# Kernel tuning notes

Measured on AMD Instinct MI355X. Metric: run time of the kernel, lower is better.

The kernel has to match this reference:

```python
import jax, jax.numpy as jnp
import numpy as np

N_NODES = 50000
N_EDGES = 800000
IN_CH = 128
HEADS = 2
OUT_CH = 64
NEG_SLOPE = 0.2


def setup_inputs() -> dict:
    key = jax.random.key(0)
    ks = jax.random.split(key, 8)
    x = jax.random.normal(ks[0], (N_NODES, IN_CH), dtype=jnp.float32)
    # edges with no self-loops (module strips them anyway before re-adding)
    src = jax.random.randint(ks[1], (N_EDGES,), 0, N_NODES)
    off = jax.random.randint(ks[2], (N_EDGES,), 1, N_NODES)
    dst = (src + off) % N_NODES
    edge_index = jnp.stack([src, dst]).astype(jnp.int64)
    sc = 1.0 / np.sqrt(IN_CH)
    Wl = jax.random.normal(ks[3], (IN_CH, HEADS * OUT_CH), dtype=jnp.float32) * sc
    att_l = jax.random.normal(ks[4], (1, HEADS, OUT_CH), dtype=jnp.float32) * 0.1
    att_r = jax.random.normal(ks[5], (1, HEADS, OUT_CH), dtype=jnp.float32) * 0.1
    Wout = jax.random.normal(ks[6], (HEADS * OUT_CH, OUT_CH), dtype=jnp.float32) * (1.0 / np.sqrt(HEADS * OUT_CH))
    bias = jnp.zeros((OUT_CH,), dtype=jnp.float32)
    return {"x": x, "edge_index": edge_index, "Wl": Wl, "att_l": att_l,
            "att_r": att_r, "Wout": Wout, "bias": bias}


def reference(x, edge_index, Wl, att_l, att_r, Wout, bias):
    N = x.shape[0]
    H, C = att_l.shape[1], att_l.shape[2]
    # input edges have no self-loops; module removes then re-adds them
    loops = jnp.arange(N, dtype=edge_index.dtype)
    src = jnp.concatenate([edge_index[0], loops])  # j (source / neighbor)
    dst = jnp.concatenate([edge_index[1], loops])  # i (target / aggregation index)
    # shared lin_l == lin_r projection -> [N, H, C]
    xh = (x @ Wl).reshape(N, H, C)
    alpha_l = jnp.sum(xh * att_l, axis=-1)  # [N, H]
    alpha_r = jnp.sum(xh * att_r, axis=-1)  # [N, H]
    # per-edge attention logits: alpha_j + alpha_i, then LeakyReLU
    e = jax.nn.leaky_relu(alpha_l[src] + alpha_r[dst], negative_slope=NEG_SLOPE)  # [E, H]
    # segment softmax over destination nodes (numerically stable)
    emax = jax.ops.segment_max(e, dst, num_segments=N)
    emax = jnp.where(jnp.isfinite(emax), emax, 0.0)
    ex = jnp.exp(e - emax[dst])
    denom = jax.ops.segment_sum(ex, dst, num_segments=N)
    alpha = ex / (denom[dst] + 1e-16)  # matches PyG softmax eps
    # weighted scatter-add aggregation of source features
    msg = xh[src] * alpha[:, :, None]                # [E, H, C]
    out = jax.ops.segment_sum(msg, dst, num_segments=N)  # [N, H, C]
    # concat heads -> output projection + bias (concat=True, bias=True path)
    out = out.reshape(N, H * C) @ Wout + bias
    return out
```

## Files before the change

### kernel.cpp

```cpp
#include <hip/hip_runtime.h>
#include <hip/hip_fp16.h>

#define NEG_SLOPE 0.2f

static __device__ __forceinline__ unsigned short f2bf(float f) {
    unsigned u = __float_as_uint(f);
    unsigned r = (u + 0x7fffu + ((u >> 16) & 1u)) >> 16;
    return (unsigned short)r;
}
static __device__ __forceinline__ float bflo(unsigned z) {
    return __uint_as_float((z & 0xffffu) << 16);
}
static __device__ __forceinline__ float bfhi(unsigned z) {
    return __uint_as_float(z & 0xffff0000u);
}

#define PREP_B 66

__global__ __launch_bounds__(256) void prep_count_kernel(
    const float* __restrict__ Wl, const float* __restrict__ Wout,
    const float* __restrict__ attL, const float* __restrict__ attR,
    float* __restrict__ Wc, float* __restrict__ avec,
    const int* __restrict__ ei, int E, int Etot, int* __restrict__ cnt)
{
    int bid = blockIdx.x;
    if (bid < PREP_B) {
        int idx = bid * 256 + threadIdx.x;
        if (idx < 128 * 128) {
            int k = idx >> 7, c = idx & 127;
            int h = c >> 6, cc = c & 63;
            const float* wl = Wl + k * 128 + h * 64;
            const float* wo = Wout + (h * 64) * 64 + cc;
            float s = 0.f;
#pragma unroll 8
            for (int m = 0; m < 64; ++m) s += wl[m] * wo[m * 64];
            Wc[k * 128 + c] = s;
        } else if (idx < 128 * 128 + 512) {
            int r = idx - 128 * 128;
            int k = r >> 2, t = r & 3;
            int h = t & 1;
            const float* av = ((t < 2) ? attL : attR) + h * 64;
            const float* wl = Wl + k * 128 + h * 64;
            float s = 0.f;
#pragma unroll 8
            for (int m = 0; m < 64; ++m) s += wl[m] * av[m];
            avec[k * 4 + t] = s;
        }
    } else {
        int e = (bid - PREP_B) * 256 + threadIdx.x;
        if (e >= Etot) return;
        int dst = (e < E) ? ei[E + e] : (e - E);
        atomicAdd(&cnt[dst], 1);
    }
}

__global__ __launch_bounds__(256, 4) void zproj_scan_kernel(
    const float* __restrict__ x, const float* __restrict__ Wc,
    const float* __restrict__ avec, int N, int ZB,
    unsigned short* __restrict__ Z, float* __restrict__ AL, float* __restrict__ AR,
    const int* __restrict__ cnt, int* __restrict__ off, int* __restrict__ chs)
{
    __shared__ float xs[64 * 136];
    __shared__ float avs[128 * 4];
    const int tid = threadIdx.x;

    if ((int)blockIdx.x >= ZB) {
        int blk = blockIdx.x - ZB;
        int* s = (int*)xs;
        int i = blk * 256 + tid;
        int v = (i < N) ? cnt[i] : 0;
        s[tid] = v; __syncthreads();
#pragma unroll
        for (int o = 1; o < 256; o <<= 1) {
            int add = (tid >= o) ? s[tid - o] : 0;
            __syncthreads();
            s[tid] += add;
            __syncthreads();
        }
        if (i < N) off[i] = s[tid] - v;
        if (tid == 255) chs[blk] = s[255];
        return;
    }

    const int row0 = blockIdx.x * 64;
    const float4* x4 = (const float4*)x;
#pragma unroll
    for (int it = 0; it < 8; ++it) {
        int f4 = it * 256 + tid;
        int r = f4 >> 5, kq = f4 & 31;
        int rsrc = row0 + r; if (rsrc >= N) rsrc = N - 1;
        float4 v = x4[(size_t)rsrc * 32 + kq];
        *(float4*)&xs[r * 136 + kq * 4] = v;
    }
    if (tid < 128) *(float4*)&avs[tid * 4] = *(const float4*)&avec[tid * 4];
    __syncthreads();

    const int cg = tid & 31;
    const int rg = tid >> 5;
    const int c0 = cg * 4, r0 = rg * 8;
    float acc[8][4] = {};
    const float* wp = Wc + c0;
    for (int kc = 0; kc < 32; ++kc) {
        int k = kc * 4;
        float4 w0 = *(const float4*)&wp[(k + 0) * 128];
        float4 w1 = *(const float4*)&wp[(k + 1) * 128];
        float4 w2 = *(const float4*)&wp[(k + 2) * 128];
        float4 w3 = *(const float4*)&wp[(k + 3) * 128];
#pragma unroll
        for (int i = 0; i < 8; ++i) {
            float4 xv = *(const float4*)&xs[(r0 + i) * 136 + k];
            acc[i][0] += xv.x * w0.x + xv.y * w1.x + xv.z * w2.x + xv.w * w3.x;
            acc[i][1] += xv.x * w0.y + xv.y * w1.y + xv.z * w2.y + xv.w * w3.y;
            acc[i][2] += xv.x * w0.z + xv.y * w1.z + xv.z * w2.z + xv.w * w3.z;
            acc[i][3] += xv.x * w0.w + xv.y * w1.w + xv.z * w2.w + xv.w * w3.w;
        }
    }
#pragma unroll
    for (int i = 0; i < 8; ++i) {
        int row = row0 + r0 + i;
        if (row < N) {
            ushort4 zz;
            zz.x = f2bf(acc[i][0]); zz.y = f2bf(acc[i][1]);
            zz.z = f2bf(acc[i][2]); zz.w = f2bf(acc[i][3]);
            *(ushort4*)(Z + (size_t)row * 128 + c0) = zz;
        }
    }
    {
        int row = tid >> 2, t = tid & 3;
        const float* xr = &xs[row * 136];
        float s = 0.f;
#pragma unroll 8
        for (int k = 0; k < 128; k += 4) {
            float4 xv = *(const float4*)&xr[k];
            s += xv.x * avs[(k + 0) * 4 + t] + xv.y * avs[(k + 1) * 4 + t]
               + xv.z * avs[(k + 2) * 4 + t] + xv.w * avs[(k + 3) * 4 + t];
        }
        int grow = row0 + row;
        if (grow < N) {
            if (t < 2) AL[grow * 2 + t] = s;
            else       AR[grow * 2 + (t - 2)] = s;
        }
    }
}

__global__ __launch_bounds__(256) void scan2(int* __restrict__ chs, int nb)
{
    __shared__ int s[256];
    int t = threadIdx.x;
    int v = (t < nb) ? chs[t] : 0;
    s[t] = v; __syncthreads();
#pragma unroll
    for (int o = 1; o < 256; o <<= 1) {
        int add = (t >= o) ? s[t - o] : 0;
        __syncthreads();
        s[t] += add;
        __syncthreads();
    }
    if (t < nb) chs[t] = s[t] - v;
}

__global__ void fill_kernel(const int* __restrict__ ei, int E, int Etot,
                            const float* __restrict__ AL, const float* __restrict__ AR,
                            int* __restrict__ off, const int* __restrict__ chs,
                            uint2* __restrict__ edg)
{
    int e = blockIdx.x * 256 + threadIdx.x;
    if (e >= Etot) return;
    int src, dst;
    if (e < E) { src = ei[e]; dst = ei[E + e]; }
    else       { src = e - E; dst = e - E; }
    float2 al = *(const float2*)&AL[src * 2];
    float2 ar = *(const float2*)&AR[dst * 2];
    float e0 = al.x + ar.x, e1 = al.y + ar.y;
    e0 = (e0 < 0.f) ? NEG_SLOPE * e0 : e0;
    e1 = (e1 < 0.f) ? NEG_SLOPE * e1 : e1;
    int pos = atomicAdd(&off[dst], 1) + chs[dst >> 8];
    __half2 hh = __floats2half2_rn(__expf(e0), __expf(e1));
    uint2 rec;
    rec.x = (unsigned)src;
    rec.y = *(unsigned*)&hh;
    edg[pos] = rec;
}

__global__ __launch_bounds__(256) void agg_kernel(
    const int* __restrict__ off, const int* __restrict__ chs,
    const int* __restrict__ cnt, const uint2* __restrict__ edg,
    const unsigned short* __restrict__ Z, const float* __restrict__ bias,
    float* __restrict__ out, int N)
{
    int wid = threadIdx.x >> 6, lane = threadIdx.x & 63;
    int node = blockIdx.x * 4 + wid;
    if (node >= N) return;
    int base = chs[node >> 8];
    int end  = base + off[node];
    int start = end - cnt[node];
    int g  = lane >> 4;
    int l4 = lane & 15;
    int h  = l4 >> 3;
    float a[8] = {};
    float ws = 0.f;
    uint2 rec = make_uint2(0u, 0u);
    if (start + g < end) rec = edg[start + g];
    for (int e = start; e < end; e += 4) {
        uint2 nrec = make_uint2(0u, 0u);
        int ne = e + 4 + g;
        if (ne < end) nrec = edg[ne];
        int j = (int)rec.x;
        unsigned hv = h ? (rec.y >> 16) : (rec.y & 0xffffu);
        float w = __half2float(__ushort_as_half((unsigned short)hv));
        uint4 zz = *(const uint4*)(Z + (size_t)j * 128 + l4 * 8);
        a[0] += w * bflo(zz.x); a[1] += w * bfhi(zz.x);
        a[2] += w * bflo(zz.y); a[3] += w * bfhi(zz.y);
        a[4] += w * bflo(zz.z); a[5] += w * bfhi(zz.z);
        a[6] += w * bflo(zz.w); a[7] += w * bfhi(zz.w);
        ws += w;
        rec = nrec;
    }
#pragma unroll
    for (int i = 0; i < 8; ++i) {
        a[i] += __shfl_xor(a[i], 16);
        a[i] += __shfl_xor(a[i], 32);
    }
    ws += __shfl_xor(ws, 16);
    ws += __shfl_xor(ws, 32);
    float inv = 1.f / (ws + 1e-16f);
#pragma unroll
    for (int i = 0; i < 8; ++i) a[i] *= inv;
#pragma unroll
    for (int i = 0; i < 8; ++i) a[i] += __shfl_xor(a[i], 8);
    if (lane < 8) {
        float4 b0 = *(const float4*)&bias[lane * 8];
        float4 b1 = *(const float4*)&bias[lane * 8 + 4];
        float4 o0 = make_float4(a[0] + b0.x, a[1] + b0.y, a[2] + b0.z, a[3] + b0.w);
        float4 o1 = make_float4(a[4] + b1.x, a[5] + b1.y, a[6] + b1.z, a[7] + b1.w);
        *(float4*)&out[(size_t)node * 64 + lane * 8] = o0;
        *(float4*)&out[(size_t)node * 64 + lane * 8 + 4] = o1;
    }
}

extern "C" void kernel_launch(void* const* d_in, const int* in_sizes, int n_in,
                              void* d_out, int out_size, void* d_ws, size_t ws_size,
                              hipStream_t stream)
{
    const float* x    = (const float*)d_in[0];
    const int*   ei   = (const int*)d_in[1];
    const float* Wl   = (const float*)d_in[2];
    const float* attL = (const float*)d_in[3];
    const float* attR = (const float*)d_in[4];
    const float* Wout = (const float*)d_in[5];
    const float* bias = (const float*)d_in[6];
    float* out = (float*)d_out;

    const int N = in_sizes[0] / 128;
    const int E = in_sizes[1] / 2;
    const int Etot = E + N;

    char* ws = (char*)d_ws;
    size_t o = 0;
    auto alloc = [&](size_t bytes) {
        void* p = ws + o; o += (bytes + 255) & ~(size_t)255; return p;
    };
    float*          Wc   = (float*)alloc(128 * 128 * 4);
    float*          AV   = (float*)alloc(128 * 4 * 4);
    unsigned short* Z    = (unsigned short*)alloc((size_t)N * 128 * 2);
    float*          AL   = (float*)alloc((size_t)N * 2 * 4);
    float*          AR   = (float*)alloc((size_t)N * 2 * 4);
    int*            CNT  = (int*)alloc((size_t)N * 4);
    int*            OFF  = (int*)alloc((size_t)N * 4);
    int*            CHS  = (int*)alloc(256 * 4);
    uint2*          EDG  = (uint2*)alloc((size_t)Etot * 8);

    hipMemsetAsync(CNT, 0, (size_t)N * 4, stream);

    int eb = (Etot + 255) / 256;
    int nb = (N + 255) / 256;
    int ZB = (N + 63) / 64;

    prep_count_kernel<<<PREP_B + eb, 256, 0, stream>>>(Wl, Wout, attL, attR,
                                                       Wc, AV, ei, E, Etot, CNT);
    zproj_scan_kernel<<<ZB + nb, 256, 0, stream>>>(x, Wc, AV, N, ZB,
                                                   Z, AL, AR, CNT, OFF, CHS);
    scan2<<<1, 256, 0, stream>>>(CHS, nb);
    fill_kernel<<<eb, 256, 0, stream>>>(ei, E, Etot, AL, AR, OFF, CHS, EDG);
    agg_kernel<<<(N + 3) / 4, 256, 0, stream>>>(OFF, CHS, CNT, EDG, Z, bias, out, N);
}
```

Before: 231.0 us.

## Two-level bucket sort of edges by destination chunk to cut atomic contention

Replaces per-node global atomics in the fill step with per-64-node chunk atomics on padded counters, then adds a sort kernel that scatters each chunk's edges to exact per-node slots using shared-memory atomics. Source index and low destination bits are packed into one record. The aggregation loop is unrolled to process two edge batches per iteration and skips zero-weight records. This adds an extra pass over the edge array and an extra buffer, and the packing limits source indices to 26 bits.

```diff
diff --git a/kernel.cpp b/kernel.cpp
--- a/kernel.cpp
+++ b/kernel.cpp
@@ -143,9 +143,13 @@
     }
 }
 
-__global__ __launch_bounds__(256) void scan2(int* __restrict__ chs, int nb)
+__global__ __launch_bounds__(256) void scan2x(
+    int* __restrict__ chs, int nb, int N, int Etot,
+    const int* __restrict__ off, int* __restrict__ chunkbase,
+    int* __restrict__ chunkptr)
 {
     __shared__ int s[256];
+    __shared__ int ex[256];
     int t = threadIdx.x;
     int v = (t < nb) ? chs[t] : 0;
     s[t] = v; __syncthreads();
@@ -156,13 +160,22 @@
         s[t] += add;
         __syncthreads();
     }
-    if (t < nb) chs[t] = s[t] - v;
-}
-
-__global__ void fill_kernel(const int* __restrict__ ei, int E, int Etot,
-                            const float* __restrict__ AL, const float* __restrict__ AR,
-                            int* __restrict__ off, const int* __restrict__ chs,
-                            uint2* __restrict__ edg)
+    int excl = s[t] - v;
+    ex[t] = excl;
+    if (t < nb) chs[t] = excl;
+    __syncthreads();
+    int C = (N + 63) >> 6;
+    for (int c = t; c <= C; c += 256) {
+        int node = c << 6;
+        int base = (node >= N) ? Etot : (ex[node >> 8] + off[node]);
+        chunkbase[c] = base;
+        if (c < C) chunkptr[c * 16] = base;
+    }
+}
+
+__global__ void fill2_kernel(const int* __restrict__ ei, int E, int Etot,
+                             const float* __restrict__ AL, const float* __restrict__ AR,
+                             int* __restrict__ chunkptr, uint2* __restrict__ edg)
 {
     int e = blockIdx.x * 256 + threadIdx.x;
     if (e >= Etot) return;
@@ -174,47 +187,83 @@
     float e0 = al.x + ar.x, e1 = al.y + ar.y;
     e0 = (e0 < 0.f) ? NEG_SLOPE * e0 : e0;
     e1 = (e1 < 0.f) ? NEG_SLOPE * e1 : e1;
-    int pos = atomicAdd(&off[dst], 1) + chs[dst >> 8];
+    int pos = atomicAdd(&chunkptr[(dst >> 6) * 16], 1);
     __half2 hh = __floats2half2_rn(__expf(e0), __expf(e1));
     uint2 rec;
-    rec.x = (unsigned)src;
+    rec.x = ((unsigned)src << 6) | (unsigned)(dst & 63);
     rec.y = *(unsigned*)&hh;
     edg[pos] = rec;
 }
 
+__global__ __launch_bounds__(256) void sort_kernel(
+    const int* __restrict__ chunkbase, const int* __restrict__ chs,
+    const int* __restrict__ off, const uint2* __restrict__ edg,
+    uint2* __restrict__ edg2, int N)
+{
+    __shared__ int ptr[64];
+    int c = blockIdx.x;
+    int t = threadIdx.x;
+    if (t < 64) {
+        int n = c * 64 + t;
+        ptr[t] = (n < N) ? (chs[n >> 8] + off[n]) : 0;
+    }
+    int base = chunkbase[c], endb = chunkbase[c + 1];
+    __syncthreads();
+    for (int i = base + t; i < endb; i += 256) {
+        uint2 r = edg[i];
+        int dlo = r.x & 63;
+        int p = atomicAdd(&ptr[dlo], 1);
+        edg2[p] = make_uint2(r.x >> 6, r.y);
+    }
+}
+
 __global__ __launch_bounds__(256) void agg_kernel(
     const int* __restrict__ off, const int* __restrict__ chs,
-    const int* __restrict__ cnt, const uint2* __restrict__ edg,
+    const int* __restrict__ cnt, const uint2* __restrict__ edg2,
     const unsigned short* __restrict__ Z, const float* __restrict__ bias,
     float* __restrict__ out, int N)
 {
     int wid = threadIdx.x >> 6, lane = threadIdx.x & 63;
     int node = blockIdx.x * 4 + wid;
     if (node >= N) return;
-    int base = chs[node >> 8];
-    int end  = base + off[node];
-    int start = end - cnt[node];
+    int start = chs[node >> 8] + off[node];
+    int end = start + cnt[node];
     int g  = lane >> 4;
     int l4 = lane & 15;
     int h  = l4 >> 3;
     float a[8] = {};
     float ws = 0.f;
-    uint2 rec = make_uint2(0u, 0u);
-    if (start + g < end) rec = edg[start + g];
-    for (int e = start; e < end; e += 4) {
-        uint2 nrec = make_uint2(0u, 0u);
-        int ne = e + 4 + g;
-        if (ne < end) nrec = edg[ne];
-        int j = (int)rec.x;
-        unsigned hv = h ? (rec.y >> 16) : (rec.y & 0xffffu);
-        float w = __half2float(__ushort_as_half((unsigned short)hv));
-        uint4 zz = *(const uint4*)(Z + (size_t)j * 128 + l4 * 8);
-        a[0] += w * bflo(zz.x); a[1] += w * bfhi(zz.x);
-        a[2] += w * bflo(zz.y); a[3] += w * bfhi(zz.y);
-        a[4] += w * bflo(zz.z); a[5] += w * bfhi(zz.z);
-        a[6] += w * bflo(zz.w); a[7] += w * bfhi(zz.w);
-        ws += w;
-        rec = nrec;
+    uint2 rA = make_uint2(0u, 0u), rB = make_uint2(0u, 0u);
+    if (start + g < end)     rA = edg2[start + g];
+    if (start + 4 + g < end) rB = edg2[start + 4 + g];
+    for (int e = start; e < end; e += 8) {
+        uint2 nA = make_uint2(0u, 0u), nB = make_uint2(0u, 0u);
+        int pa = e + 8 + g, pb = e + 12 + g;
+        if (pa < end) nA = edg2[pa];
+        if (pb < end) nB = edg2[pb];
+        if (rA.y) {
+            int j = (int)rA.x;
+            unsigned hv = h ? (rA.y >> 16) : (rA.y & 0xffffu);
+            float w = __half2float(__ushort_as_half((unsigned short)hv));
+            uint4 zz = *(const uint4*)(Z + (size_t)j * 128 + l4 * 8);
+            a[0] += w * bflo(zz.x); a[1] += w * bfhi(zz.x);
+            a[2] += w * bflo(zz.y); a[3] += w * bfhi(zz.y);
+            a[4] += w * bflo(zz.z); a[5] += w * bfhi(zz.z);
+            a[6] += w * bflo(zz.w); a[7] += w * bfhi(zz.w);
+            ws += w;
+        }
+        if (rB.y) {
+            int j = (int)rB.x;
+            unsigned hv = h ? (rB.y >> 16) : (rB.y & 0xffffu);
+            float w = __half2float(__ushort_as_half((unsigned short)hv));
+            uint4 zz = *(const uint4*)(Z + (size_t)j * 128 + l4 * 8);
+            a[0] += w * bflo(zz.x); a[1] += w * bfhi(zz.x);
+            a[2] += w * bflo(zz.y); a[3] += w * bfhi(zz.y);
+            a[4] += w * bflo(zz.z); a[5] += w * bfhi(zz.z);
+            a[6] += w * bflo(zz.w); a[7] += w * bfhi(zz.w);
+            ws += w;
+        }
+        rA = nA; rB = nB;
     }
 #pragma unroll
     for (int i = 0; i < 8; ++i) {
@@ -254,21 +303,25 @@
     const int N = in_sizes[0] / 128;
     const int E = in_sizes[1] / 2;
     const int Etot = E + N;
+    const int C = (N + 63) >> 6;
 
     char* ws = (char*)d_ws;
     size_t o = 0;
     auto alloc = [&](size_t bytes) {
         void* p = ws + o; o += (bytes + 255) & ~(size_t)255; return p;
     };
-    float*          Wc   = (float*)alloc(128 * 128 * 4);
-    float*          AV   = (float*)alloc(128 * 4 * 4);
-    unsigned short* Z    = (unsigned short*)alloc((size_t)N * 128 * 2);
-    float*          AL   = (float*)alloc((size_t)N * 2 * 4);
-    float*          AR   = (float*)alloc((size_t)N * 2 * 4);
-    int*            CNT  = (int*)alloc((size_t)N * 4);
-    int*            OFF  = (int*)alloc((size_t)N * 4);
-    int*            CHS  = (int*)alloc(256 * 4);
-    uint2*          EDG  = (uint2*)alloc((size_t)Etot * 8);
+    float*          Wc    = (float*)alloc(128 * 128 * 4);
+    float*          AV    = (float*)alloc(128 * 4 * 4);
+    unsigned short* Z     = (unsigned short*)alloc((size_t)N * 128 * 2);
+    float*          AL    = (float*)alloc((size_t)N * 2 * 4);
+    float*          AR    = (float*)alloc((size_t)N * 2 * 4);
+    int*            CNT   = (int*)alloc((size_t)N * 4);
+    int*            OFF   = (int*)alloc((size_t)N * 4);
+    int*            CHS   = (int*)alloc(256 * 4);
+    int*            CBASE = (int*)alloc((size_t)(C + 1) * 4);
+    int*            CPTR  = (int*)alloc((size_t)C * 16 * 4);
+    uint2*          EDG   = (uint2*)alloc((size_t)Etot * 8);
+    uint2*          EDG2  = (uint2*)alloc((size_t)Etot * 8);
 
     hipMemsetAsync(CNT, 0, (size_t)N * 4, stream);
 
@@ -280,7 +333,8 @@
                                                        Wc, AV, ei, E, Etot, CNT);
     zproj_scan_kernel<<<ZB + nb, 256, 0, stream>>>(x, Wc, AV, N, ZB,
                                                    Z, AL, AR, CNT, OFF, CHS);
-    scan2<<<1, 256, 0, stream>>>(CHS, nb);
-    fill_kernel<<<eb, 256, 0, stream>>>(ei, E, Etot, AL, AR, OFF, CHS, EDG);
-    agg_kernel<<<(N + 3) / 4, 256, 0, stream>>>(OFF, CHS, CNT, EDG, Z, bias, out, N);
-}
+    scan2x<<<1, 256, 0, stream>>>(CHS, nb, N, Etot, OFF, CBASE, CPTR);
+    fill2_kernel<<<eb, 256, 0, stream>>>(ei, E, Etot, AL, AR, CPTR, EDG);
+    sort_kernel<<<C, 256, 0, stream>>>(CBASE, CHS, OFF, EDG, EDG2, N);
+    agg_kernel<<<(N + 3) / 4, 256, 0, stream>>>(OFF, CHS, CNT, EDG2, Z, bias, out, N);
+}
```

Result: slower. 262.9 us (+13.8%).

## Move edge attention weight computation from fill into aggregation kernel

Applied to the files above, without the earlier changes.

The fill kernel now writes only the source index per sorted edge instead of a (src, fp16 exp-weights) record. The aggregation kernel gathers AL for each source and AR for the node, then computes leaky-relu and exp itself. Its edge loop is also unrolled to process two groups of four edges per iteration, with source indices prefetched one iteration ahead. This halves the edge-list write and read traffic and removes the random AL/AR gathers from fill. In exchange, agg does an extra random AL gather per edge and recomputes exp per lane, and the weights are now kept in fp32 instead of fp16.

```diff
diff --git a/kernel.cpp b/kernel.cpp
--- a/kernel.cpp
+++ b/kernel.cpp
@@ -1,5 +1,4 @@
 #include <hip/hip_runtime.h>
-#include <hip/hip_fp16.h>
 
 #define NEG_SLOPE 0.2f
 
@@ -160,61 +159,65 @@
 }
 
 __global__ void fill_kernel(const int* __restrict__ ei, int E, int Etot,
-                            const float* __restrict__ AL, const float* __restrict__ AR,
                             int* __restrict__ off, const int* __restrict__ chs,
-                            uint2* __restrict__ edg)
+                            int* __restrict__ srcs)
 {
     int e = blockIdx.x * 256 + threadIdx.x;
     if (e >= Etot) return;
     int src, dst;
     if (e < E) { src = ei[e]; dst = ei[E + e]; }
     else       { src = e - E; dst = e - E; }
-    float2 al = *(const float2*)&AL[src * 2];
-    float2 ar = *(const float2*)&AR[dst * 2];
-    float e0 = al.x + ar.x, e1 = al.y + ar.y;
-    e0 = (e0 < 0.f) ? NEG_SLOPE * e0 : e0;
-    e1 = (e1 < 0.f) ? NEG_SLOPE * e1 : e1;
     int pos = atomicAdd(&off[dst], 1) + chs[dst >> 8];
-    __half2 hh = __floats2half2_rn(__expf(e0), __expf(e1));
-    uint2 rec;
-    rec.x = (unsigned)src;
-    rec.y = *(unsigned*)&hh;
-    edg[pos] = rec;
+    srcs[pos] = src;
 }
 
 __global__ __launch_bounds__(256) void agg_kernel(
     const int* __restrict__ off, const int* __restrict__ chs,
-    const int* __restrict__ cnt, const uint2* __restrict__ edg,
+    const int* __restrict__ cnt, const int* __restrict__ srcs,
+    const float* __restrict__ AL, const float* __restrict__ AR,
     const unsigned short* __restrict__ Z, const float* __restrict__ bias,
     float* __restrict__ out, int N)
 {
     int wid = threadIdx.x >> 6, lane = threadIdx.x & 63;
     int node = blockIdx.x * 4 + wid;
     if (node >= N) return;
-    int base = chs[node >> 8];
-    int end  = base + off[node];
+    int end = chs[node >> 8] + off[node];
     int start = end - cnt[node];
     int g  = lane >> 4;
     int l4 = lane & 15;
     int h  = l4 >> 3;
+    float arh = AR[node * 2 + h];
     float a[8] = {};
     float ws = 0.f;
-    uint2 rec = make_uint2(0u, 0u);
-    if (start + g < end) rec = edg[start + g];
-    for (int e = start; e < end; e += 4) {
-        uint2 nrec = make_uint2(0u, 0u);
-        int ne = e + 4 + g;
-        if (ne < end) nrec = edg[ne];
-        int j = (int)rec.x;
-        unsigned hv = h ? (rec.y >> 16) : (rec.y & 0xffffu);
-        float w = __half2float(__ushort_as_half((unsigned short)hv));
-        uint4 zz = *(const uint4*)(Z + (size_t)j * 128 + l4 * 8);
-        a[0] += w * bflo(zz.x); a[1] += w * bfhi(zz.x);
-        a[2] += w * bflo(zz.y); a[3] += w * bfhi(zz.y);
-        a[4] += w * bflo(zz.z); a[5] += w * bfhi(zz.z);
-        a[6] += w * bflo(zz.w); a[7] += w * bfhi(zz.w);
-        ws += w;
-        rec = nrec;
+    int last = end - 1;
+    int sA = srcs[min(start + g, last)];
+    int sB = srcs[min(start + 4 + g, last)];
+    for (int e = start; e < end; e += 8) {
+        int nsA = srcs[min(e + 8 + g, last)];
+        int nsB = srcs[min(e + 12 + g, last)];
+        {
+            float al = AL[sA * 2 + h];
+            float t = al + arh; t = (t < 0.f) ? NEG_SLOPE * t : t;
+            float w = ((e + g) < end) ? __expf(t) : 0.f;
+            uint4 zz = *(const uint4*)(Z + (size_t)sA * 128 + l4 * 8);
+            a[0] += w * bflo(zz.x); a[1] += w * bfhi(zz.x);
+            a[2] += w * bflo(zz.y); a[3] += w * bfhi(zz.y);
+            a[4] += w * bflo(zz.z); a[5] += w * bfhi(zz.z);
+            a[6] += w * bflo(zz.w); a[7] += w * bfhi(zz.w);
+            ws += w;
+        }
+        {
+            float al = AL[sB * 2 + h];
+            float t = al + arh; t = (t < 0.f) ? NEG_SLOPE * t : t;
+            float w = ((e + 4 + g) < end) ? __expf(t) : 0.f;
+            uint4 zz = *(const uint4*)(Z + (size_t)sB * 128 + l4 * 8);
+            a[0] += w * bflo(zz.x); a[1] += w * bfhi(zz.x);
+            a[2] += w * bflo(zz.y); a[3] += w * bfhi(zz.y);
+            a[4] += w * bflo(zz.z); a[5] += w * bfhi(zz.z);
+            a[6] += w * bflo(zz.w); a[7] += w * bfhi(zz.w);
+            ws += w;
+        }
+        sA = nsA; sB = nsB;
     }
 #pragma unroll
     for (int i = 0; i < 8; ++i) {
@@ -268,7 +271,7 @@
     int*            CNT  = (int*)alloc((size_t)N * 4);
     int*            OFF  = (int*)alloc((size_t)N * 4);
     int*            CHS  = (int*)alloc(256 * 4);
-    uint2*          EDG  = (uint2*)alloc((size_t)Etot * 8);
+    int*            SRCS = (int*)alloc((size_t)Etot * 4);
 
     hipMemsetAsync(CNT, 0, (size_t)N * 4, stream);
 
@@ -281,6 +284,7 @@
     zproj_scan_kernel<<<ZB + nb, 256, 0, stream>>>(x, Wc, AV, N, ZB,
                                                    Z, AL, AR, CNT, OFF, CHS);
     scan2<<<1, 256, 0, stream>>>(CHS, nb);
-    fill_kernel<<<eb, 256, 0, stream>>>(ei, E, Etot, AL, AR, OFF, CHS, EDG);
-    agg_kernel<<<(N + 3) / 4, 256, 0, stream>>>(OFF, CHS, CNT, EDG, Z, bias, out, N);
-}
+    fill_kernel<<<eb, 256, 0, stream>>>(ei, E, Etot, OFF, CHS, SRCS);
+    agg_kernel<<<(N + 3) / 4, 256, 0, stream>>>(OFF, CHS, CNT, SRCS,
+                                                AL, AR, Z, bias, out, N);
+}
```

After: 239.5 us. 3.7% more time.
